# Performance work log

Measured on AMD Instinct MI355X. Metric: run time of the kernel, lower is better.

Reference implementation:

```python
import jax, jax.numpy as jnp
import numpy as np

MAXDISP = 48


def setup_inputs() -> dict:
    key = jax.random.key(0)
    k1, k2 = jax.random.split(key)
    B, C, H, W = 4, 32, 64, 128
    x = jax.random.normal(k1, (B, C, H, W), dtype=jnp.float32)
    y = jax.random.normal(k2, (B, C, H, W), dtype=jnp.float32)
    return {"x": x, "y": y}


def reference(x, y):
    # cost[b, :C, d, h, w]   = x[b, :, h, w]     if w >= d else 0
    # cost[b, C:, d, h, w]   = y[b, :, h, w - d] if w >= d else 0
    B, C, H, W = x.shape
    D = MAXDISP
    d = jnp.arange(D)[:, None]            # [D, 1]
    w = jnp.arange(W)[None, :]            # [1, W]
    mask = (w >= d)                       # [D, W]
    mask_b = mask[None, None, :, None, :] # [1, 1, D, 1, W]

    # left features: broadcast over D, mask out w < d
    x_part = jnp.where(mask_b, x[:, :, None, :, :], 0.0)  # [B, C, D, H, W]

    # right features: gather shifted columns w - d (clipped), then mask
    y_idx = jnp.maximum(w - d, 0)                         # [D, W]
    y_g = jnp.take(y, y_idx, axis=3)                      # [B, C, H, D, W]
    y_g = jnp.transpose(y_g, (0, 1, 3, 2, 4))             # [B, C, D, H, W]
    y_part = jnp.where(mask_b, y_g, 0.0)

    return jnp.concatenate([x_part, y_part], axis=1)      # [B, 2C, D, H, W]
```

## Files before the change

### kernel.cpp

```cpp
#include <hip/hip_runtime.h>


typedef float f4_native __attribute__((ext_vector_type(4)));

__global__ __launch_bounds__(256) void cost_volume_kernel(
    const float* __restrict__ x, const float* __restrict__ y,
    f4_native* __restrict__ out)
{
    const int t    = threadIdx.x;
    const int w4   = t & 31;
    const int w0   = w4 << 2;
    const int hsub = t >> 5;

    const int g = blockIdx.x;
    const int h = ((g & 7) << 3) + hsub;
    int q = g >> 3;
    const int d = q % 48;
    q = q / 48;
    const int cc = q & 63;
    const int b  = q >> 6;

    float4 v;
    if (cc < 32) {
        v = *(const float4*)(x + (((b * 32 + cc) * 64 + h) << 7) + w0);
    } else {
        const float4 cur =
            *(const float4*)(y + (((b * 32 + (cc - 32)) * 64 + h) << 7) + w0);
        const int s = d >> 2;
        const int r = d & 3;
        float4 c2, p2;
        c2.x = __shfl_up(cur.x, s, 32);
        c2.y = __shfl_up(cur.y, s, 32);
        c2.z = __shfl_up(cur.z, s, 32);
        c2.w = __shfl_up(cur.w, s, 32);
        p2.x = __shfl_up(cur.x, s + 1, 32);
        p2.y = __shfl_up(cur.y, s + 1, 32);
        p2.z = __shfl_up(cur.z, s + 1, 32);
        p2.w = __shfl_up(cur.w, s + 1, 32);
        switch (r) {
            case 0:  v = c2; break;
            case 1:  v = make_float4(p2.w, c2.x, c2.y, c2.z); break;
            case 2:  v = make_float4(p2.z, p2.w, c2.x, c2.y); break;
            default: v = make_float4(p2.y, p2.z, p2.w, c2.x); break;
        }
    }
    v.x = (w0 + 0 >= d) ? v.x : 0.0f;
    v.y = (w0 + 1 >= d) ? v.y : 0.0f;
    v.z = (w0 + 2 >= d) ? v.z : 0.0f;
    v.w = (w0 + 3 >= d) ? v.w : 0.0f;

    f4_native vn;
    vn.x = v.x; vn.y = v.y; vn.z = v.z; vn.w = v.w;
    __builtin_nontemporal_store(vn, &out[g * 256 + t]);
}

extern "C" void kernel_launch(void* const* d_in, const int* in_sizes, int n_in,
                              void* d_out, int out_size, void* d_ws, size_t ws_size,
                              hipStream_t stream) {
    const float* x = (const float*)d_in[0];
    const float* y = (const float*)d_in[1];
    f4_native* out = (f4_native*)d_out;

    const int block = 256;
    const int grid  = 98304;
    cost_volume_kernel<<<grid, block, 0, stream>>>(x, y, out);
}
```

Before: 429.6 us.

## Process four disparities and all rows per block to reuse loaded inputs

Each block now covers one (b, channel) slice and a group of four disparities across all 64 rows. Every input row is loaded once into registers and written out four times, and one pair of shuffles serves all four disparities because they share a shift. This cuts the grid from 98304 to 3072 blocks and reduces per-output index math and input loads. The non-temporal store hint is also dropped in favour of plain float4 stores, which may change cache behaviour on this store-bound output.

After: 401.3 us. 6.6% less time.

```diff
diff --git a/kernel.cpp b/kernel.cpp
--- a/kernel.cpp
+++ b/kernel.cpp
@@ -1,57 +1,77 @@
 #include <hip/hip_runtime.h>
 
 
-typedef float f4_native __attribute__((ext_vector_type(4)));
-
 __global__ __launch_bounds__(256) void cost_volume_kernel(
     const float* __restrict__ x, const float* __restrict__ y,
-    f4_native* __restrict__ out)
+    float4* __restrict__ out)
 {
     const int t    = threadIdx.x;
     const int w4   = t & 31;
     const int w0   = w4 << 2;
     const int hsub = t >> 5;
 
-    const int g = blockIdx.x;
-    const int h = ((g & 7) << 3) + hsub;
-    int q = g >> 3;
-    const int d = q % 48;
-    q = q / 48;
-    const int cc = q & 63;
-    const int b  = q >> 6;
+    const int bid = blockIdx.x;
+    const int dg  = bid % 12;
+    const int q   = bid / 12;
+    const int cc  = q & 63;
+    const int b   = q >> 6;
+    const int d0  = dg << 2;
 
-    float4 v;
+    float4* outp = out + (((b * 64 + cc) * 48 + d0) * 2048 + t);
+
+    float4 c2[8], p2[8];
     if (cc < 32) {
-        v = *(const float4*)(x + (((b * 32 + cc) * 64 + h) << 7) + w0);
+        const float* xp = x + (((b * 32 + cc) * 64 + hsub) << 7) + w0;
+#pragma unroll
+        for (int ho = 0; ho < 8; ++ho)
+            c2[ho] = *(const float4*)(xp + (ho << 10));
+#pragma unroll
+        for (int j = 0; j < 4; ++j) {
+            const int d = d0 + j;
+#pragma unroll
+            for (int ho = 0; ho < 8; ++ho) {
+                float4 v = c2[ho];
+                v.x = (w0 + 0 >= d) ? v.x : 0.0f;
+                v.y = (w0 + 1 >= d) ? v.y : 0.0f;
+                v.z = (w0 + 2 >= d) ? v.z : 0.0f;
+                v.w = (w0 + 3 >= d) ? v.w : 0.0f;
+                outp[j * 2048 + ho * 256] = v;
+            }
+        }
     } else {
-        const float4 cur =
-            *(const float4*)(y + (((b * 32 + (cc - 32)) * 64 + h) << 7) + w0);
-        const int s = d >> 2;
-        const int r = d & 3;
-        float4 c2, p2;
-        c2.x = __shfl_up(cur.x, s, 32);
-        c2.y = __shfl_up(cur.y, s, 32);
-        c2.z = __shfl_up(cur.z, s, 32);
-        c2.w = __shfl_up(cur.w, s, 32);
-        p2.x = __shfl_up(cur.x, s + 1, 32);
-        p2.y = __shfl_up(cur.y, s + 1, 32);
-        p2.z = __shfl_up(cur.z, s + 1, 32);
-        p2.w = __shfl_up(cur.w, s + 1, 32);
-        switch (r) {
-            case 0:  v = c2; break;
-            case 1:  v = make_float4(p2.w, c2.x, c2.y, c2.z); break;
-            case 2:  v = make_float4(p2.z, p2.w, c2.x, c2.y); break;
-            default: v = make_float4(p2.y, p2.z, p2.w, c2.x); break;
+        const float* yp = y + (((b * 32 + (cc - 32)) * 64 + hsub) << 7) + w0;
+#pragma unroll
+        for (int ho = 0; ho < 8; ++ho) {
+            const float4 yv = *(const float4*)(yp + (ho << 10));
+            c2[ho].x = __shfl_up(yv.x, dg, 32);
+            c2[ho].y = __shfl_up(yv.y, dg, 32);
+            c2[ho].z = __shfl_up(yv.z, dg, 32);
+            c2[ho].w = __shfl_up(yv.w, dg, 32);
+            p2[ho].x = __shfl_up(yv.x, dg + 1, 32);
+            p2[ho].y = __shfl_up(yv.y, dg + 1, 32);
+            p2[ho].z = __shfl_up(yv.z, dg + 1, 32);
+            p2[ho].w = __shfl_up(yv.w, dg + 1, 32);
+        }
+#pragma unroll
+        for (int j = 0; j < 4; ++j) {
+            const int d = d0 + j;
+#pragma unroll
+            for (int ho = 0; ho < 8; ++ho) {
+                float4 v;
+                switch (j) {
+                    case 0:  v = c2[ho]; break;
+                    case 1:  v = make_float4(p2[ho].w, c2[ho].x, c2[ho].y, c2[ho].z); break;
+                    case 2:  v = make_float4(p2[ho].z, p2[ho].w, c2[ho].x, c2[ho].y); break;
+                    default: v = make_float4(p2[ho].y, p2[ho].z, p2[ho].w, c2[ho].x); break;
+                }
+                v.x = (w0 + 0 >= d) ? v.x : 0.0f;
+                v.y = (w0 + 1 >= d) ? v.y : 0.0f;
+                v.z = (w0 + 2 >= d) ? v.z : 0.0f;
+                v.w = (w0 + 3 >= d) ? v.w : 0.0f;
+                outp[j * 2048 + ho * 256] = v;
+            }
         }
     }
-    v.x = (w0 + 0 >= d) ? v.x : 0.0f;
-    v.y = (w0 + 1 >= d) ? v.y : 0.0f;
-    v.z = (w0 + 2 >= d) ? v.z : 0.0f;
-    v.w = (w0 + 3 >= d) ? v.w : 0.0f;
-
-    f4_native vn;
-    vn.x = v.x; vn.y = v.y; vn.z = v.z; vn.w = v.w;
-    __builtin_nontemporal_store(vn, &out[g * 256 + t]);
 }
 
 extern "C" void kernel_launch(void* const* d_in, const int* in_sizes, int n_in,
@@ -59,9 +79,9 @@
                               hipStream_t stream) {
     const float* x = (const float*)d_in[0];
     const float* y = (const float*)d_in[1];
-    f4_native* out = (f4_native*)d_out;
+    float4* out = (float4*)d_out;
 
     const int block = 256;
-    const int grid  = 98304;
+    const int grid  = 4 * 64 * 12;
     cost_volume_kernel<<<grid, block, 0, stream>>>(x, y, out);
 }
```

## Switch to grid-stride loop with fewer blocks and regular stores

Applied to the files above, without the earlier changes.

Shrinks the launch from one block per 256 float4 outputs to 2048 blocks. Each thread now loops 48 times over a grid-stride index with an unroll of 4, which amortises block launch and index setup. The nontemporal store is replaced by an ordinary float4 store, which may change cache behaviour on this write-bound 200MB output. Loads may be less parallel per thread, since each iteration's global load feeds a shuffle.

Result: no change. 428.0 us (-0.4%).

```diff
diff --git a/kernel.cpp b/kernel.cpp
--- a/kernel.cpp
+++ b/kernel.cpp
@@ -1,57 +1,55 @@
 #include <hip/hip_runtime.h>
 
 
-typedef float f4_native __attribute__((ext_vector_type(4)));
-
 __global__ __launch_bounds__(256) void cost_volume_kernel(
     const float* __restrict__ x, const float* __restrict__ y,
-    f4_native* __restrict__ out)
+    float4* __restrict__ out)
 {
-    const int t    = threadIdx.x;
-    const int w4   = t & 31;
-    const int w0   = w4 << 2;
-    const int hsub = t >> 5;
+    const int tid = blockIdx.x * 256 + threadIdx.x;
 
-    const int g = blockIdx.x;
-    const int h = ((g & 7) << 3) + hsub;
-    int q = g >> 3;
-    const int d = q % 48;
-    q = q / 48;
-    const int cc = q & 63;
-    const int b  = q >> 6;
+#pragma unroll 4
+    for (int k = 0; k < 48; ++k) {
+        const int i  = k * 524288 + tid;
+        const int w4 = i & 31;
+        const int w0 = w4 << 2;
+        const int h  = (i >> 5) & 63;
+        const int sl = i >> 11;
+        const int d  = sl % 48;
+        const int q  = sl / 48;
+        const int cc = q & 63;
+        const int b  = q >> 6;
 
-    float4 v;
-    if (cc < 32) {
-        v = *(const float4*)(x + (((b * 32 + cc) * 64 + h) << 7) + w0);
-    } else {
-        const float4 cur =
-            *(const float4*)(y + (((b * 32 + (cc - 32)) * 64 + h) << 7) + w0);
-        const int s = d >> 2;
-        const int r = d & 3;
-        float4 c2, p2;
-        c2.x = __shfl_up(cur.x, s, 32);
-        c2.y = __shfl_up(cur.y, s, 32);
-        c2.z = __shfl_up(cur.z, s, 32);
-        c2.w = __shfl_up(cur.w, s, 32);
-        p2.x = __shfl_up(cur.x, s + 1, 32);
-        p2.y = __shfl_up(cur.y, s + 1, 32);
-        p2.z = __shfl_up(cur.z, s + 1, 32);
-        p2.w = __shfl_up(cur.w, s + 1, 32);
-        switch (r) {
-            case 0:  v = c2; break;
-            case 1:  v = make_float4(p2.w, c2.x, c2.y, c2.z); break;
-            case 2:  v = make_float4(p2.z, p2.w, c2.x, c2.y); break;
-            default: v = make_float4(p2.y, p2.z, p2.w, c2.x); break;
+        float4 v;
+        if (cc < 32) {
+            v = *(const float4*)(x + (((b * 32 + cc) * 64 + h) << 7) + w0);
+        } else {
+            const float4 yv =
+                *(const float4*)(y + (((b * 32 + (cc - 32)) * 64 + h) << 7) + w0);
+            const int s = d >> 2;
+            const int r = d & 3;
+            float4 c2, p2;
+            c2.x = __shfl_up(yv.x, s, 32);
+            c2.y = __shfl_up(yv.y, s, 32);
+            c2.z = __shfl_up(yv.z, s, 32);
+            c2.w = __shfl_up(yv.w, s, 32);
+            p2.x = __shfl_up(yv.x, s + 1, 32);
+            p2.y = __shfl_up(yv.y, s + 1, 32);
+            p2.z = __shfl_up(yv.z, s + 1, 32);
+            p2.w = __shfl_up(yv.w, s + 1, 32);
+            switch (r) {
+                case 0:  v = c2; break;
+                case 1:  v = make_float4(p2.w, c2.x, c2.y, c2.z); break;
+                case 2:  v = make_float4(p2.z, p2.w, c2.x, c2.y); break;
+                default: v = make_float4(p2.y, p2.z, p2.w, c2.x); break;
+            }
         }
+        v.x = (w0 + 0 >= d) ? v.x : 0.0f;
+        v.y = (w0 + 1 >= d) ? v.y : 0.0f;
+        v.z = (w0 + 2 >= d) ? v.z : 0.0f;
+        v.w = (w0 + 3 >= d) ? v.w : 0.0f;
+
+        out[i] = v;
     }
-    v.x = (w0 + 0 >= d) ? v.x : 0.0f;
-    v.y = (w0 + 1 >= d) ? v.y : 0.0f;
-    v.z = (w0 + 2 >= d) ? v.z : 0.0f;
-    v.w = (w0 + 3 >= d) ? v.w : 0.0f;
-
-    f4_native vn;
-    vn.x = v.x; vn.y = v.y; vn.z = v.z; vn.w = v.w;
-    __builtin_nontemporal_store(vn, &out[g * 256 + t]);
 }
 
 extern "C" void kernel_launch(void* const* d_in, const int* in_sizes, int n_in,
@@ -59,9 +57,9 @@
                               hipStream_t stream) {
     const float* x = (const float*)d_in[0];
     const float* y = (const float*)d_in[1];
-    f4_native* out = (f4_native*)d_out;
+    float4* out = (float4*)d_out;
 
     const int block = 256;
-    const int grid  = 98304;
+    const int grid  = 2048;
     cost_volume_kernel<<<grid, block, 0, stream>>>(x, y, out);
 }
```
